# Optimization experiments

Hardware: AMD Instinct MI355X
Metric: run time of the kernel (lower is better)

## Reference

```python
import jax, jax.numpy as jnp
import numpy as np

N_NODES = 50000
N_EDGES = 1200000
IN_FEATS = 64
OUT_FEATS = 64
NEG_SLOPE = 0.01  # F.leaky_relu default


def setup_inputs() -> dict:
    key = jax.random.key(0)
    k1, k2, k3, k4, k5, k6 = jax.random.split(key, 6)
    feature = jax.random.normal(k1, (N_NODES, IN_FEATS), dtype=jnp.float32)
    attn_w = jax.random.normal(k2, (2 * IN_FEATS, 1), dtype=jnp.float32) * 0.1
    lin_w = jax.random.normal(k3, (OUT_FEATS, 2 * IN_FEATS), dtype=jnp.float32) * 0.1
    lin_b = jax.random.normal(k4, (OUT_FEATS,), dtype=jnp.float32) * 0.1
    src = jax.random.randint(k5, (N_EDGES,), 0, N_NODES, dtype=jnp.int32)
    dst = jax.random.randint(k6, (N_EDGES,), 0, N_NODES, dtype=jnp.int32)
    return {"feature": feature, "attn_w": attn_w, "lin_w": lin_w,
            "lin_b": lin_b, "src": src, "dst": dst}


def reference(feature, attn_w, lin_w, lin_b, src, dst):
    N = feature.shape[0]
    # edge attention: leaky_relu(attn_fc([h_src, h_dst]))
    # split attn weight to avoid materializing the [E, 2*in] concat
    a_src, a_dst = attn_w[:IN_FEATS, 0], attn_w[IN_FEATS:, 0]
    e = jax.nn.leaky_relu(feature[src] @ a_src + feature[dst] @ a_dst,
                          negative_slope=NEG_SLOPE)  # [E]
    # segment softmax over incoming edges of each destination node
    emax = jax.ops.segment_max(e, dst, num_segments=N)
    emax = jnp.where(jnp.isfinite(emax), emax, 0.0)  # guard empty segments
    ex = jnp.exp(e - emax[dst])                       # [E]
    denom = jax.ops.segment_sum(ex, dst, num_segments=N)          # [N]
    num = jax.ops.segment_sum(ex[:, None] * feature[src], dst,
                              num_segments=N)                      # [N, in]
    hm = jnp.where(denom[:, None] > 0, num / denom[:, None], 0.0)
    # node apply: relu(Linear([h, hm]))
    h = jnp.concatenate([feature, hm], axis=1) @ lin_w.T + lin_b
    return jax.nn.relu(h)
```

## Files before the change

### kernel.cpp

```cpp
#include <hip/hip_runtime.h>
#include <math.h>

#define N_NODES 50000
#define N_EDGES 1200000
#define F 64
#define CAP 49
#define BSTR2 56
#define OVF_MAX 1024
#define NBIN 782
#define BSTR 16
#define CAP_BIN 2304
#define TILE 8192
#define NTILE ((N_EDGES + TILE - 1) / TILE)
#define XSTR 72
#define PSTR 68

typedef __attribute__((ext_vector_type(8))) short short8;
typedef __attribute__((ext_vector_type(4))) float v4f;


__device__ __forceinline__ unsigned short f32_to_bf16_rne(float f) {
    unsigned u = __float_as_uint(f);
    return (unsigned short)((u + 0x7FFFu + ((u >> 16) & 1u)) >> 16);
}

__global__ void k_prep(const float* __restrict__ feature,
                       const float* __restrict__ attn_w,
                       const float* __restrict__ lin_w,
                       float* __restrict__ s, float* __restrict__ dd,
                       unsigned short* __restrict__ fb,
                       unsigned* __restrict__ fq32,
                       unsigned short* __restrict__ wq) {
    int gid = blockIdx.x * blockDim.x + threadIdx.x;
    if (gid < 64 * 128) wq[gid] = f32_to_bf16_rne(lin_w[gid]);
    int wave = gid >> 6;
    int lane = threadIdx.x & 63;
    if (wave >= N_NODES) return;
    float f = feature[wave * F + lane];
    fb[wave * F + lane] = f32_to_bf16_rne(f);
    if (lane < 16) {
        float4 x = ((const float4*)(feature + (size_t)wave * F))[lane];
        int pk0 = __builtin_amdgcn_cvt_pk_fp8_f32(x.x, x.y, 0, false);
        int pkw = __builtin_amdgcn_cvt_pk_fp8_f32(x.z, x.w, pk0, true);
        fq32[wave * 16 + lane] = (unsigned)pkw;
    }
    float sv = f * attn_w[lane];
    float dv = f * attn_w[F + lane];
    #pragma unroll
    for (int o = 32; o > 0; o >>= 1) {
        sv += __shfl_down(sv, o, 64);
        dv += __shfl_down(dv, o, 64);
    }
    if (lane == 0) {
        s[wave] = sv;
        dd[wave] = dv;
    }
}

__global__ __launch_bounds__(256) void k_bin(
        const int* __restrict__ src, const int* __restrict__ dst,
        int* __restrict__ bin_cnt, unsigned* __restrict__ binned) {
    __shared__ unsigned ord[TILE];
    __shared__ int cnt_l[NBIN], off_l[NBIN], cur_l[NBIN], base_g[NBIN];
    __shared__ int buf[256];
    int t = threadIdx.x;
    int e0 = blockIdx.x * TILE;
    int ecnt = N_EDGES - e0; if (ecnt > TILE) ecnt = TILE;
    for (int i = t; i < NBIN; i += 256) cnt_l[i] = 0;
    __syncthreads();
    int n4 = ecnt >> 2;
    const int4* s4p = (const int4*)src + (e0 >> 2);
    const int4* d4p = (const int4*)dst + (e0 >> 2);
    unsigned pk[32];
    int ng = 0;
    #pragma unroll
    for (int k = 0; k < 8; k++) {
        int c = t + k * 256;
        if (c < n4) {
            int4 d4 = d4p[c];
            int4 s4 = s4p[c];
            pk[4 * k + 0] = (((unsigned)d4.x) << 16) | (unsigned)s4.x;
            pk[4 * k + 1] = (((unsigned)d4.y) << 16) | (unsigned)s4.y;
            pk[4 * k + 2] = (((unsigned)d4.z) << 16) | (unsigned)s4.z;
            pk[4 * k + 3] = (((unsigned)d4.w) << 16) | (unsigned)s4.w;
            atomicAdd(&cnt_l[pk[4 * k + 0] >> 22], 1);
            atomicAdd(&cnt_l[pk[4 * k + 1] >> 22], 1);
            atomicAdd(&cnt_l[pk[4 * k + 2] >> 22], 1);
            atomicAdd(&cnt_l[pk[4 * k + 3] >> 22], 1);
            ng = k + 1;
        }
    }
    __syncthreads();
    int c0[4];
    int sum = 0;
    #pragma unroll
    for (int j = 0; j < 4; j++) {
        int idx = t * 4 + j;
        c0[j] = (idx < NBIN) ? cnt_l[idx] : 0;
        sum += c0[j];
    }
    buf[t] = sum;
    __syncthreads();
    #pragma unroll
    for (int d = 1; d < 256; d <<= 1) {
        int x = (t >= d) ? buf[t - d] : 0;
        __syncthreads();
        buf[t] += x;
        __syncthreads();
    }
    int excl = buf[t] - sum;
    #pragma unroll
    for (int j = 0; j < 4; j++) {
        int idx = t * 4 + j;
        if (idx < NBIN) {
            off_l[idx] = excl;
            cur_l[idx] = excl;
        }
        excl += c0[j];
    }
    int rot = (int)((blockIdx.x * 389u) % NBIN);
    for (int i = t; i < NBIN; i += 256) {
        int idx = i + rot; if (idx >= NBIN) idx -= NBIN;
        base_g[idx] = atomicAdd(&bin_cnt[idx * BSTR], cnt_l[idx]);
    }
    __syncthreads();
    for (int k = 0; k < ng; k++) {
        #pragma unroll
        for (int u = 0; u < 4; u++) {
            unsigned v = pk[4 * k + u];
            int r = atomicAdd(&cur_l[v >> 22], 1);
            ord[r] = v;
        }
    }
    __syncthreads();
    for (int i = t; i < ecnt; i += 256) {
        unsigned v = ord[i];
        int b = v >> 22;
        int pos = base_g[b] + (i - off_l[b]);
        if (pos < CAP_BIN) binned[(size_t)b * CAP_BIN + pos] = v;
    }
}

__global__ __launch_bounds__(256, 4) void k_fused(
        const unsigned* __restrict__ binned, const int* __restrict__ bin_cnt,
        int* __restrict__ cnt, unsigned short* __restrict__ bucket,
        int* __restrict__ ovf_cnt, unsigned* __restrict__ ovf,
        const float* __restrict__ s, const float* __restrict__ dd,
        const unsigned short* __restrict__ fb, const unsigned* __restrict__ fq32,
        const unsigned short* __restrict__ wq, const float* __restrict__ lin_b,
        float* __restrict__ out) {
    __shared__ int cnt_l[64];
    __shared__ __align__(16) unsigned short buck_l[64 * BSTR2];
    __shared__ __align__(16) unsigned short xl[4][16][XSTR];
    __shared__ __align__(16) float p_l[4][16][PSTR];
    int t = threadIdx.x;
    int wid = t >> 6, lane = t & 63;
    int bin = blockIdx.x;
    int n0 = bin << 6;
    int nn = N_NODES - n0; if (nn > 64) nn = 64;
    if (t < 64) cnt_l[t] = 0;
    {
        uint4 z4 = {0, 0, 0, 0};
        uint4* b4 = (uint4*)buck_l;
        for (int i = t; i < 448; i += 256) b4[i] = z4;
    }
    __syncthreads();
    int E = bin_cnt[bin * BSTR];
    if (E > CAP_BIN) E = CAP_BIN;
    const unsigned* be = binned + (size_t)bin * CAP_BIN;
    for (int i = t; i < E; i += 256) {
        unsigned v = be[i];
        int local = (v >> 16) & 63;
        int sid = (int)(v & 0xFFFFu);
        int r = atomicAdd(&cnt_l[local], 1);
        if (r < CAP) {
            buck_l[local * BSTR2 + r] = (unsigned short)sid;
        } else {
            int o = atomicAdd(ovf_cnt, 1);
            if (o < OVF_MAX)
                ovf[o] = ((unsigned)(n0 + local) << 16) | (unsigned)sid;
        }
    }
    __syncthreads();
    if (t < nn) {
        cnt[n0 + t] = cnt_l[t];
        if (cnt_l[t] > CAP) {
            for (int k2 = 0; k2 < CAP; k2++)
                bucket[(size_t)(n0 + t) * CAP + k2] = buck_l[t * BSTR2 + k2];
        }
    }
    __syncthreads();
    #pragma unroll 2
    for (int j = 0; j < 16; j++) {
        int local = wid * 16 + j;
        int dg = cnt_l[local];
        if (dg > CAP) dg = 0;
        float pr = 0.0f;
        if (lane < dg) {
            int si = (int)buck_l[local * BSTR2 + lane];
            float v = s[si] + dd[n0 + local];
            v = v > 0.0f ? v : 0.01f * v;
            pr = __expf(v);
        }
        float l = pr;
        #pragma unroll
        for (int o = 32; o > 0; o >>= 1)
            l += __shfl_xor(l, o, 64);
        p_l[wid][j][lane] = pr * __builtin_amdgcn_rcpf(l + 1e-30f);
    }
    int grp = lane >> 4;
    int c16 = lane & 15;
    unsigned wvN[8];
    float pwN[8];
    {
        int local = wid * 16;
        ushort4 skA = *(const ushort4*)&buck_l[local * BSTR2 + grp * 8];
        ushort4 skB = *(const ushort4*)&buck_l[local * BSTR2 + grp * 8 + 4];
        float4 pA = *(const float4*)&p_l[wid][0][grp * 8];
        float4 pB = *(const float4*)&p_l[wid][0][grp * 8 + 4];
        int sk[8] = {skA.x, skA.y, skA.z, skA.w, skB.x, skB.y, skB.z, skB.w};
        #pragma unroll
        for (int u = 0; u < 8; u++) wvN[u] = fq32[sk[u] * 16 + c16];
        pwN[0] = pA.x; pwN[1] = pA.y; pwN[2] = pA.z; pwN[3] = pA.w;
        pwN[4] = pB.x; pwN[5] = pB.y; pwN[6] = pB.z; pwN[7] = pB.w;
    }
    #pragma unroll
    for (int j = 0; j < 16; j++) {
        unsigned wvC[8];
        float pwC[8];
        #pragma unroll
        for (int u = 0; u < 8; u++) { wvC[u] = wvN[u]; pwC[u] = pwN[u]; }
        if (j + 1 < 16) {
            int local = wid * 16 + j + 1;
            ushort4 skA = *(const ushort4*)&buck_l[local * BSTR2 + grp * 8];
            ushort4 skB = *(const ushort4*)&buck_l[local * BSTR2 + grp * 8 + 4];
            float4 pA = *(const float4*)&p_l[wid][j + 1][grp * 8];
            float4 pB = *(const float4*)&p_l[wid][j + 1][grp * 8 + 4];
            int sk[8] = {skA.x, skA.y, skA.z, skA.w,
                         skB.x, skB.y, skB.z, skB.w};
            #pragma unroll
            for (int u = 0; u < 8; u++) wvN[u] = fq32[sk[u] * 16 + c16];
            pwN[0] = pA.x; pwN[1] = pA.y; pwN[2] = pA.z; pwN[3] = pA.w;
            pwN[4] = pB.x; pwN[5] = pB.y; pwN[6] = pB.z; pwN[7] = pB.w;
        }
        float a0 = 0.0f, a1 = 0.0f, a2 = 0.0f, a3 = 0.0f;
        #pragma unroll
        for (int u = 0; u < 8; u++) {
            a0 = fmaf(pwC[u], __builtin_amdgcn_cvt_f32_fp8(wvC[u], 0), a0);
            a1 = fmaf(pwC[u], __builtin_amdgcn_cvt_f32_fp8(wvC[u], 1), a1);
            a2 = fmaf(pwC[u], __builtin_amdgcn_cvt_f32_fp8(wvC[u], 2), a2);
            a3 = fmaf(pwC[u], __builtin_amdgcn_cvt_f32_fp8(wvC[u], 3), a3);
        }
        int dgj = cnt_l[wid * 16 + j];
        if (dgj > 32 && dgj <= CAP) {
            int local = wid * 16 + j;
            ushort4 skA = *(const ushort4*)&buck_l[local * BSTR2 + 32 + grp * 8];
            ushort4 skB = *(const ushort4*)&buck_l[local * BSTR2 + 36 + grp * 8];
            float4 pA = *(const float4*)&p_l[wid][j][32 + grp * 8];
            float4 pB = *(const float4*)&p_l[wid][j][36 + grp * 8];
            int sk[8] = {skA.x, skA.y, skA.z, skA.w,
                         skB.x, skB.y, skB.z, skB.w};
            unsigned wv2[8];
            #pragma unroll
            for (int u = 0; u < 8; u++) wv2[u] = fq32[sk[u] * 16 + c16];
            float pw2[8] = {pA.x, pA.y, pA.z, pA.w, pB.x, pB.y, pB.z, pB.w};
            #pragma unroll
            for (int u = 0; u < 8; u++) {
                a0 = fmaf(pw2[u], __builtin_amdgcn_cvt_f32_fp8(wv2[u], 0), a0);
                a1 = fmaf(pw2[u], __builtin_amdgcn_cvt_f32_fp8(wv2[u], 1), a1);
                a2 = fmaf(pw2[u], __builtin_amdgcn_cvt_f32_fp8(wv2[u], 2), a2);
                a3 = fmaf(pw2[u], __builtin_amdgcn_cvt_f32_fp8(wv2[u], 3), a3);
            }
        }
        a0 += __shfl_xor(a0, 16, 64); a0 += __shfl_xor(a0, 32, 64);
        a1 += __shfl_xor(a1, 16, 64); a1 += __shfl_xor(a1, 32, 64);
        a2 += __shfl_xor(a2, 16, 64); a2 += __shfl_xor(a2, 32, 64);
        a3 += __shfl_xor(a3, 16, 64); a3 += __shfl_xor(a3, 32, 64);
        if (lane < 16) {
            ushort4 st;
            st.x = f32_to_bf16_rne(a0);
            st.y = f32_to_bf16_rne(a1);
            st.z = f32_to_bf16_rne(a2);
            st.w = f32_to_bf16_rne(a3);
            *(ushort4*)&xl[wid][j][c16 * 4] = st;
        }
    }
    int n0w = n0 + wid * 16;
    if (n0w >= N_NODES) return;
    int m = lane & 15, quad = lane >> 4;
    short8 afr[4];
    #pragma unroll
    for (int ks = 0; ks < 2; ks++) {
        int kb = ks * 32 + quad * 8;
        afr[ks] = *(const short8*)&fb[(size_t)(n0w + m) * F + kb];
    }
    #pragma unroll
    for (int ks = 2; ks < 4; ks++) {
        int kb = (ks - 2) * 32 + quad * 8;
        afr[ks] = *(const short8*)&xl[wid][m][kb];
    }
    #pragma unroll
    for (int nt = 0; nt < 4; nt++) {
        v4f acc = {0.0f, 0.0f, 0.0f, 0.0f};
        #pragma unroll
        for (int ks = 0; ks < 4; ks++) {
            int kb = ks * 32 + quad * 8;
            short8 b = *(const short8*)&wq[(nt * 16 + m) * 128 + kb];
            acc = __builtin_amdgcn_mfma_f32_16x16x32_bf16(afr[ks], b, acc,
                                                          0, 0, 0);
        }
        int colo = nt * 16 + m;
        float bias = lin_b[colo];
        #pragma unroll
        for (int r = 0; r < 4; r++) {
            int row = quad * 4 + r;
            float v = acc[r] + bias;
            out[(size_t)(n0w + row) * F + colo] = fmaxf(v, 0.0f);
        }
    }
}

__global__ __launch_bounds__(256) void k_cleanup(
        const unsigned short* __restrict__ bucket,
        const int* __restrict__ cnt,
        const int* __restrict__ ovf_cnt, const unsigned int* __restrict__ ovf,
        const float* __restrict__ s, const float* __restrict__ dd,
        const float* __restrict__ feature,
        const float* __restrict__ lin_w, const float* __restrict__ lin_b,
        float* __restrict__ out) {
    int M = *ovf_cnt;
    if (M > OVF_MAX) M = OVF_MAX;
    if (M == 0) return;
    __shared__ float Wl[64 * 129];
    __shared__ int list[128];
    __shared__ int nlist;
    __shared__ unsigned short edg[4][256];
    __shared__ float xc[4][128];
    int t = threadIdx.x;
    for (int i = t; i < 64 * 128; i += 256)
        Wl[(i >> 7) * 129 + (i & 127)] = lin_w[i];
    if (t == 0) {
        nlist = 0;
        for (int i = 0; i < M; i++) {
            int d = (int)(ovf[i] >> 16);
            bool seen = false;
            for (int j = 0; j < nlist; j++) if (list[j] == d) seen = true;
            if (!seen && nlist < 128) list[nlist++] = d;
        }
    }
    __syncthreads();
    int wid = t >> 6, lane = t & 63;
    for (int idx = wid; idx < nlist; idx += 4) {
        int n = list[idx];
        int deg = cnt[n];
        if (lane < CAP) edg[wid][lane] = bucket[n * CAP + lane];
        int k2 = CAP;
        for (int base = 0; base < M; base += 64) {
            int i2 = base + lane;
            unsigned val = 0;
            bool mt = false;
            if (i2 < M) { val = ovf[i2]; mt = ((int)(val >> 16) == n); }
            unsigned long long mask = __ballot(mt);
            if (mt) {
                int pos = k2 + __popcll(mask & ((1ULL << lane) - 1ULL));
                if (pos < 256) edg[wid][pos] = (unsigned short)(val & 0xFFFFu);
            }
            k2 += __popcll(mask);
        }
        __threadfence_block();
        int nd = deg < 256 ? deg : 256;
        float m = -1e30f, l = 0.0f, acc = 0.0f;
        float dn = dd[n];
        for (int c0 = 0; c0 < nd; c0 += 64) {
            int j = c0 + lane;
            int sid = 0;
            float ev = -1e30f;
            if (j < nd) {
                sid = (int)edg[wid][j];
                float v = s[sid] + dn;
                ev = v > 0.0f ? v : 0.01f * v;
            }
            float cm = ev;
            #pragma unroll
            for (int o = 32; o > 0; o >>= 1)
                cm = fmaxf(cm, __shfl_xor(cm, o, 64));
            float np = (j < nd) ? __expf(ev - cm) : 0.0f;
            float cl = np;
            #pragma unroll
            for (int o = 32; o > 0; o >>= 1)
                cl += __shfl_xor(cl, o, 64);
            float cacc = 0.0f;
            int c = nd - c0; if (c > 64) c = 64;
            for (int k = 0; k < c; k += 16) {
                float fvv[16];
                #pragma unroll
                for (int u = 0; u < 16; u++) {
                    int sk = __builtin_amdgcn_readlane(sid, k + u);
                    fvv[u] = feature[sk * F + lane];
                }
                #pragma unroll
                for (int u = 0; u < 16; u++) {
                    float pk = __uint_as_float(
                        __builtin_amdgcn_readlane(__float_as_uint(np), k + u));
                    cacc = fmaf(pk, fvv[u], cacc);
                }
            }
            float mn = fmaxf(m, cm);
            float sc = __expf(m - mn);
            float sc2 = __expf(cm - mn);
            l = l * sc + cl * sc2;
            acc = acc * sc + cacc * sc2;
            m = mn;
        }
        float hm = acc / l;
        xc[wid][lane] = feature[n * F + lane];
        xc[wid][64 + lane] = hm;
        __threadfence_block();
        float oa = lin_b[lane];
        #pragma unroll
        for (int k = 0; k < 128; k++)
            oa += xc[wid][k] * Wl[lane * 129 + k];
        out[n * F + lane] = fmaxf(oa, 0.0f);
    }
}

extern "C" void kernel_launch(void* const* d_in, const int* in_sizes, int n_in,
                              void* d_out, int out_size, void* d_ws, size_t ws_size,
                              hipStream_t stream) {
    const float* feature = (const float*)d_in[0];
    const float* attn_w  = (const float*)d_in[1];
    const float* lin_w   = (const float*)d_in[2];
    const float* lin_b   = (const float*)d_in[3];
    const int*   src     = (const int*)d_in[4];
    const int*   dst     = (const int*)d_in[5];
    float* out = (float*)d_out;
    char* ws = (char*)d_ws;

    float*          s       = (float*)(ws);
    float*          dd      = (float*)(ws + 200000);
    int*            cnt     = (int*)  (ws + 400000);
    int*            bin_cnt = (int*)  (ws + 600000);
    int*            ovf_cnt = (int*)  (ws + 650048);
    unsigned*       ovf     = (unsigned*)(ws + 650112);
    unsigned short* bucket  = (unsigned short*)(ws + 654208);
    unsigned*       binned  = (unsigned*)(ws + 5554208);
    unsigned short* fb      = (unsigned short*)(ws + 12761120);
    unsigned*       fq32    = (unsigned*)(ws + 19161120);
    unsigned short* wq      = (unsigned short*)(ws + 22361120);

    hipMemsetAsync(ws + 600000, 0, 50112, stream);
    k_prep<<<(N_NODES * 64) / 256, 256, 0, stream>>>(
        feature, attn_w, lin_w, s, dd, fb, fq32, wq);
    k_bin<<<NTILE, 256, 0, stream>>>(src, dst, bin_cnt, binned);
    k_fused<<<NBIN, 256, 0, stream>>>(
        binned, bin_cnt, cnt, bucket, ovf_cnt, ovf, s, dd, fb, fq32,
        wq, lin_b, out);
    k_cleanup<<<1, 256, 0, stream>>>(
        bucket, cnt, ovf_cnt, ovf, s, dd, feature, lin_w, lin_b, out);
}
```

Before: 139.5 us.

## Shrink bin tile, vectorize prep to four nodes per wave, fold memset

The edge-binning tile shrinks from 8192 to 2368 edges, so k_bin launches many more blocks with smaller shared buffers and per-thread register arrays. This is meant to improve parallelism and occupancy during binning. k_prep now handles four nodes per wave using float4 loads, 16-lane xor reductions and vectorized bf16 stores, cutting its launch to a quarter of the blocks. It also zeroes the bin and overflow counters itself, which removes the separate hipMemsetAsync. The trade-off is more per-tile global atomics and prefix work in k_bin.

```diff
diff --git a/kernel.cpp b/kernel.cpp
--- a/kernel.cpp
+++ b/kernel.cpp
@@ -10,7 +10,7 @@
 #define NBIN 782
 #define BSTR 16
 #define CAP_BIN 2304
-#define TILE 8192
+#define TILE 2368
 #define NTILE ((N_EDGES + TILE - 1) / TILE)
 #define XSTR 72
 #define PSTR 68
@@ -30,30 +30,38 @@
                        float* __restrict__ s, float* __restrict__ dd,
                        unsigned short* __restrict__ fb,
                        unsigned* __restrict__ fq32,
-                       unsigned short* __restrict__ wq) {
+                       unsigned short* __restrict__ wq,
+                       int* __restrict__ bin_cnt, int* __restrict__ ovf_cnt) {
     int gid = blockIdx.x * blockDim.x + threadIdx.x;
     if (gid < 64 * 128) wq[gid] = f32_to_bf16_rne(lin_w[gid]);
-    int wave = gid >> 6;
+    if (gid < NBIN * BSTR) bin_cnt[gid] = 0;
+    if (gid == NBIN * BSTR) *ovf_cnt = 0;
+    int wv = gid >> 6;
     int lane = threadIdx.x & 63;
-    if (wave >= N_NODES) return;
-    float f = feature[wave * F + lane];
-    fb[wave * F + lane] = f32_to_bf16_rne(f);
-    if (lane < 16) {
-        float4 x = ((const float4*)(feature + (size_t)wave * F))[lane];
-        int pk0 = __builtin_amdgcn_cvt_pk_fp8_f32(x.x, x.y, 0, false);
-        int pkw = __builtin_amdgcn_cvt_pk_fp8_f32(x.z, x.w, pk0, true);
-        fq32[wave * 16 + lane] = (unsigned)pkw;
-    }
-    float sv = f * attn_w[lane];
-    float dv = f * attn_w[F + lane];
-    #pragma unroll
-    for (int o = 32; o > 0; o >>= 1) {
-        sv += __shfl_down(sv, o, 64);
-        dv += __shfl_down(dv, o, 64);
-    }
-    if (lane == 0) {
-        s[wave] = sv;
-        dd[wave] = dv;
+    int sub = lane >> 4, c = lane & 15;
+    int node = wv * 4 + sub;
+    float4 x = ((const float4*)feature)[node * 16 + c];
+    float4 wa = ((const float4*)attn_w)[c];
+    float4 wd = ((const float4*)attn_w)[16 + c];
+    float sv = x.x * wa.x + x.y * wa.y + x.z * wa.z + x.w * wa.w;
+    float dv = x.x * wd.x + x.y * wd.y + x.z * wd.z + x.w * wd.w;
+    #pragma unroll
+    for (int o = 8; o > 0; o >>= 1) {
+        sv += __shfl_xor(sv, o, 64);
+        dv += __shfl_xor(dv, o, 64);
+    }
+    ushort4 fbv;
+    fbv.x = f32_to_bf16_rne(x.x);
+    fbv.y = f32_to_bf16_rne(x.y);
+    fbv.z = f32_to_bf16_rne(x.z);
+    fbv.w = f32_to_bf16_rne(x.w);
+    ((ushort4*)fb)[node * 16 + c] = fbv;
+    int pk0 = __builtin_amdgcn_cvt_pk_fp8_f32(x.x, x.y, 0, false);
+    int pkw = __builtin_amdgcn_cvt_pk_fp8_f32(x.z, x.w, pk0, true);
+    fq32[node * 16 + c] = (unsigned)pkw;
+    if (c == 0) {
+        s[node] = sv;
+        dd[node] = dv;
     }
 }
 
@@ -71,10 +79,10 @@
     int n4 = ecnt >> 2;
     const int4* s4p = (const int4*)src + (e0 >> 2);
     const int4* d4p = (const int4*)dst + (e0 >> 2);
-    unsigned pk[32];
+    unsigned pk[12];
     int ng = 0;
     #pragma unroll
-    for (int k = 0; k < 8; k++) {
+    for (int k = 0; k < 3; k++) {
         int c = t + k * 256;
         if (c < n4) {
             int4 d4 = d4p[c];
@@ -448,9 +456,8 @@
     unsigned*       fq32    = (unsigned*)(ws + 19161120);
     unsigned short* wq      = (unsigned short*)(ws + 22361120);
 
-    hipMemsetAsync(ws + 600000, 0, 50112, stream);
-    k_prep<<<(N_NODES * 64) / 256, 256, 0, stream>>>(
-        feature, attn_w, lin_w, s, dd, fb, fq32, wq);
+    k_prep<<<3125, 256, 0, stream>>>(
+        feature, attn_w, lin_w, s, dd, fb, fq32, wq, bin_cnt, ovf_cnt);
     k_bin<<<NTILE, 256, 0, stream>>>(src, dst, bin_cnt, binned);
     k_fused<<<NBIN, 256, 0, stream>>>(
         binned, bin_cnt, cnt, bucket, ovf_cnt, ovf, s, dd, fb, fq32,
```

After: 140.0 us. About the same (+0.3%).
